# Kernel tuning notes

Measured on AMD Instinct MI355X. Metric: run time of the kernel, lower is better.

The kernel has to match this reference:

```python
import jax, jax.numpy as jnp
import numpy as np

NEG_SLOPE = 0.2

def gat_conv(x, edge_index, W, att_src, att_dst, bias, heads, out_dim):
    """PyG-style GATConv with add_self_loops=True, concat=True.
    x: [N, F_in]; edge_index: [2, E] with row 0 = src, row 1 = dst.
    W: [F_in, heads*out_dim]; att_src/att_dst: [heads, out_dim]; bias: [heads*out_dim].
    """
    N = x.shape[0]
    loop = jnp.arange(N)
    src = jnp.concatenate([edge_index[0], loop])  # [E+N]
    dst = jnp.concatenate([edge_index[1], loop])

    h = (x @ W).reshape(N, heads, out_dim)              # [N, H, D]
    a_s = jnp.sum(h * att_src[None], axis=-1)           # [N, H]
    a_d = jnp.sum(h * att_dst[None], axis=-1)           # [N, H]

    e = a_s[src] + a_d[dst]                             # [E+N, H]
    e = jax.nn.leaky_relu(e, NEG_SLOPE)
    # segment softmax over incoming edges of each dst node
    e_max = jax.ops.segment_max(e, dst, num_segments=N)  # [N, H]
    ex = jnp.exp(e - e_max[dst])
    denom = jax.ops.segment_sum(ex, dst, num_segments=N)  # [N, H] (>0: self loops)
    alpha = ex / denom[dst]                              # [E+N, H]

    msg = h[src] * alpha[..., None]                      # [E+N, H, D]
    out = jax.ops.segment_sum(msg, dst, num_segments=N)  # [N, H, D]
    return out.reshape(N, heads * out_dim) + bias


def setup_inputs() -> dict:
    key = jax.random.key(0)
    ks = jax.random.split(key, 16)
    N, F_in, D, H = 50000, 165, 64, 4
    E = 800000
    x = jax.random.normal(ks[0], (N, F_in), dtype=jnp.float32)
    edge_index = jax.random.randint(ks[1], (2, E), 0, N, dtype=jnp.int64)

    def glorot(k, shape):
        lim = float(np.sqrt(6.0 / (shape[0] + shape[-1])))
        return jax.random.uniform(k, shape, jnp.float32, -lim, lim)

    return {
        "x": x,
        "edge_index": edge_index,
        "proj_W": glorot(ks[2], (F_in, D)),
        "proj_b": jnp.zeros((D,), jnp.float32),
        "W1": glorot(ks[3], (D, H * D)),
        "att_src1": glorot(ks[4], (H, D)),
        "att_dst1": glorot(ks[5], (H, D)),
        "b1": jnp.zeros((H * D,), jnp.float32),
        "W2": glorot(ks[6], (H * D, D)),
        "att_src2": glorot(ks[7], (1, D)),
        "att_dst2": glorot(ks[8], (1, D)),
        "b2": jnp.zeros((D,), jnp.float32),
        "cls_W": glorot(ks[9], (D, 1)),
        "cls_b": jnp.zeros((1,), jnp.float32),
    }


def reference(x, edge_index, proj_W, proj_b, W1, att_src1, att_dst1, b1,
              W2, att_src2, att_dst2, b2, cls_W, cls_b):
    D = proj_W.shape[1]
    h = jax.nn.relu(x @ proj_W + proj_b)                              # [N, 64]
    h = jax.nn.relu(gat_conv(h, edge_index, W1, att_src1, att_dst1, b1, 4, D))   # [N, 256]
    h = jax.nn.relu(gat_conv(h, edge_index, W2, att_src2, att_dst2, b2, 1, D))   # [N, 64]
    return jnp.squeeze(h @ cls_W + cls_b, axis=-1)                    # [N]
```

## Files before the change

### kernel.cpp

```cpp
#include <hip/hip_runtime.h>

#define F_IN 165
#define KP_PROJ 168
constexpr float NEG_SLOPE = 0.2f;

__global__ void k_trans(const float* __restrict__ pw, const float* __restrict__ w2,
                        const float* __restrict__ w1, const float* __restrict__ as1w,
                        const float* __restrict__ ad1w,
                        float* __restrict__ t0, float* __restrict__ t2,
                        float* __restrict__ va) {
    int i = blockIdx.x * 256 + threadIdx.x;
    const int n0 = 64 * KP_PROJ, n2 = 64 * 256;
    if (i < n0) {
        int c = i / KP_PROJ, r = i - c * KP_PROJ;
        t0[i] = (r < F_IN) ? pw[r * 64 + c] : 0.f;
    } else if (i < n0 + n2) {
        int j = i - n0; int c = j >> 8, r = j & 255;
        t2[j] = w2[r * 64 + c];
    } else if (i < n0 + n2 + 512) {
        int j = i - n0 - n2;
        int i2 = j >> 6;
        int plane = i2 >> 2, h = i2 & 3, k = j & 63;
        const float* att = plane ? ad1w : as1w;
        float acc = 0.f;
        for (int c = 0; c < 64; ++c)
            acc = fmaf(w1[k * 256 + h * 64 + c], att[h * 64 + c], acc);
        va[j] = acc;
    }
}

__global__ void k_proj(const float* __restrict__ x, const float* __restrict__ Wt,
                       const float* __restrict__ b, float* __restrict__ h0, int N) {
    __shared__ float xs[32][KP_PROJ];
    int base = blockIdx.x * 32;
    int t = threadIdx.x;
    for (int idx = t; idx < 32 * KP_PROJ; idx += 256) {
        int nl = idx / KP_PROJ, k = idx - nl * KP_PROJ;
        int node = base + nl;
        xs[nl][k] = (node < N && k < F_IN) ? x[(size_t)node * F_IN + k] : 0.f;
    }
    __syncthreads();
    int g = t >> 6, col = t & 63;
    float acc[8];
    float bb = b[col];
#pragma unroll
    for (int m = 0; m < 8; ++m) acc[m] = bb;
    const float* wrow = Wt + col * KP_PROJ;
    for (int k4 = 0; k4 < KP_PROJ / 4; ++k4) {
        float4 wv = *(const float4*)(wrow + k4 * 4);
#pragma unroll
        for (int m = 0; m < 8; ++m) {
            float4 av = *(const float4*)&xs[g * 8 + m][k4 * 4];
            acc[m] = fmaf(av.x, wv.x, acc[m]);
            acc[m] = fmaf(av.y, wv.y, acc[m]);
            acc[m] = fmaf(av.z, wv.z, acc[m]);
            acc[m] = fmaf(av.w, wv.w, acc[m]);
        }
    }
#pragma unroll
    for (int m = 0; m < 8; ++m) {
        int node = base + g * 8 + m;
        if (node < N) h0[(size_t)node * 64 + col] = fmaxf(acc[m], 0.f);
    }
}

__global__ void k_attv1(const float* __restrict__ h0, const float* __restrict__ va,
                        float* __restrict__ as_, float* __restrict__ ad_, int N) {
    int t = threadIdx.x, lane = t & 63, wv = t >> 6;
    int n = blockIdx.x * 4 + wv;
    if (n >= N) return;
    float hv = h0[(size_t)n * 64 + lane];
    float r0 = hv * va[0 * 64 + lane], r1 = hv * va[1 * 64 + lane];
    float r2 = hv * va[2 * 64 + lane], r3 = hv * va[3 * 64 + lane];
    float r4 = hv * va[4 * 64 + lane], r5 = hv * va[5 * 64 + lane];
    float r6 = hv * va[6 * 64 + lane], r7 = hv * va[7 * 64 + lane];
#pragma unroll
    for (int off = 32; off; off >>= 1) {
        r0 += __shfl_xor(r0, off, 64); r1 += __shfl_xor(r1, off, 64);
        r2 += __shfl_xor(r2, off, 64); r3 += __shfl_xor(r3, off, 64);
        r4 += __shfl_xor(r4, off, 64); r5 += __shfl_xor(r5, off, 64);
        r6 += __shfl_xor(r6, off, 64); r7 += __shfl_xor(r7, off, 64);
    }
    if (lane == 0) {
        *(float4*)(as_ + (size_t)n * 4) = make_float4(r0, r1, r2, r3);
        *(float4*)(ad_ + (size_t)n * 4) = make_float4(r4, r5, r6, r7);
    }
}

__global__ void k_lin2(const float* __restrict__ h1, const float* __restrict__ Wt,
                       const float* __restrict__ att_s, const float* __restrict__ att_d,
                       float* __restrict__ out, float* __restrict__ as_,
                       float* __restrict__ ad_, int N) {
    __shared__ float hs[32][256];
    int base = blockIdx.x * 32;
    int t = threadIdx.x;
    for (int i = 0; i < 8; ++i) {
        int idx4 = t + i * 256;
        int nl = idx4 >> 6, k4 = idx4 & 63;
        int node = base + nl;
        float4 v = make_float4(0.f, 0.f, 0.f, 0.f);
        if (node < N) v = *(const float4*)(h1 + (size_t)node * 256 + k4 * 4);
        *(float4*)&hs[nl][k4 * 4] = v;
    }
    __syncthreads();
    int g = t >> 6, col = t & 63;
    float acc[8] = {};
    const float* wrow = Wt + col * 256;
    for (int k4 = 0; k4 < 64; ++k4) {
        float4 wv = *(const float4*)(wrow + k4 * 4);
#pragma unroll
        for (int m = 0; m < 8; ++m) {
            float4 av = *(const float4*)&hs[g * 8 + m][k4 * 4];
            acc[m] = fmaf(av.x, wv.x, acc[m]);
            acc[m] = fmaf(av.y, wv.y, acc[m]);
            acc[m] = fmaf(av.z, wv.z, acc[m]);
            acc[m] = fmaf(av.w, wv.w, acc[m]);
        }
    }
    float sw = att_s[col], dw = att_d[col];
#pragma unroll
    for (int m = 0; m < 8; ++m) {
        int node = base + g * 8 + m;
        if (node < N) out[(size_t)node * 64 + col] = acc[m];
        float sv = acc[m] * sw, dv = acc[m] * dw;
#pragma unroll
        for (int off = 32; off; off >>= 1) {
            sv += __shfl_xor(sv, off, 64);
            dv += __shfl_xor(dv, off, 64);
        }
        if (col == 0 && node < N) { as_[node] = sv; ad_[node] = dv; }
    }
}

__global__ void k_deg(const int* __restrict__ ei, int E, int N, int* __restrict__ deg) {
    int total = E + N;
    for (int i = blockIdx.x * blockDim.x + threadIdx.x; i < total; i += gridDim.x * blockDim.x) {
        int dst = (i < E) ? ei[E + i] : (i - E);
        atomicAdd(&deg[dst], 1);
    }
}

__global__ void k_scan_part(const int* __restrict__ deg, int* __restrict__ out,
                            int* __restrict__ partials, int n) {
    __shared__ int tmp[1024];
    int b = blockIdx.x, t = threadIdx.x;
    int i = b * 1024 + t;
    int v = (i < n) ? deg[i] : 0;
    tmp[t] = v;
    __syncthreads();
    for (int off = 1; off < 1024; off <<= 1) {
        int xval = (t >= off) ? tmp[t - off] : 0;
        __syncthreads();
        tmp[t] += xval;
        __syncthreads();
    }
    if (i < n) out[i] = tmp[t] - v;
    if (t == 1023) partials[b] = tmp[t];
}

__global__ void k_scan_small(int* __restrict__ partials, int nblk) {
    int lane = threadIdx.x & 63;
    int carry = 0;
    for (int base = 0; base < nblk; base += 64) {
        int idx = base + lane;
        int v = (idx < nblk) ? partials[idx] : 0;
        int orig = v;
#pragma unroll
        for (int off = 1; off < 64; off <<= 1) {
            int u = __shfl_up(v, off, 64);
            if (lane >= off) v += u;
        }
        if (idx < nblk) partials[idx] = carry + v - orig;
        carry += __shfl(v, 63, 64);
    }
}

__global__ void k_scan_add(int* __restrict__ rowptr, const int* __restrict__ partials,
                           int n, int total) {
    int i = blockIdx.x * 1024 + threadIdx.x;
    if (i < n) rowptr[i] += partials[blockIdx.x];
    if (i == 0) rowptr[n] = total;
}

__global__ void k_scatter(const int* __restrict__ ei, int E, int N,
                          const int* __restrict__ rowptr, int* __restrict__ cursor,
                          int* __restrict__ csrc) {
    int total = E + N;
    for (int i = blockIdx.x * blockDim.x + threadIdx.x; i < total; i += gridDim.x * blockDim.x) {
        int src, dst;
        if (i < E) { src = ei[i]; dst = ei[E + i]; }
        else { src = i - E; dst = i - E; }
        int pos = rowptr[dst] + atomicAdd(&cursor[dst], 1);
        csrc[pos] = src;
    }
}

__global__ void k_gat1f(const float* __restrict__ h0, const float* __restrict__ as1,
                        const float* __restrict__ ad1, const int* __restrict__ rowptr,
                        const int* __restrict__ csrc, const float* __restrict__ W1,
                        const float* __restrict__ b1, float* __restrict__ h1out, int N) {
    __shared__ float agg[4][256];
    int t = threadIdx.x, wv = t >> 6, lane = t & 63;
    int slot = lane >> 4, sl = lane & 15;
    int d = blockIdx.x * 4 + wv;
    if (d < N) {
        int s0 = rowptr[d], e0 = rowptr[d + 1];
        float4 ad = *(const float4*)(ad1 + (size_t)d * 4);
        float a00=0,a01=0,a02=0,a03=0;
        float a10=0,a11=0,a12=0,a13=0;
        float a20=0,a21=0,a22=0,a23=0;
        float a30=0,a31=0,a32=0,a33=0;
        float d0=0,d1=0,d2=0,d3=0;
        const float* hb = h0 + sl * 4;
        for (int j = s0 + slot; j < e0; j += 4) {
            int s = csrc[j];
            float4 a = *(const float4*)(as1 + (size_t)s * 4);
            float4 hv = *(const float4*)(hb + (size_t)s * 64);
            float z0 = a.x + ad.x, z1 = a.y + ad.y, z2 = a.z + ad.z, z3 = a.w + ad.w;
            z0 = (z0 > 0.f) ? z0 : NEG_SLOPE * z0;
            z1 = (z1 > 0.f) ? z1 : NEG_SLOPE * z1;
            z2 = (z2 > 0.f) ? z2 : NEG_SLOPE * z2;
            z3 = (z3 > 0.f) ? z3 : NEG_SLOPE * z3;
            float wx = __expf(z0), wy = __expf(z1), wz = __expf(z2), ww = __expf(z3);
            a00 = fmaf(wx, hv.x, a00); a01 = fmaf(wx, hv.y, a01);
            a02 = fmaf(wx, hv.z, a02); a03 = fmaf(wx, hv.w, a03);
            a10 = fmaf(wy, hv.x, a10); a11 = fmaf(wy, hv.y, a11);
            a12 = fmaf(wy, hv.z, a12); a13 = fmaf(wy, hv.w, a13);
            a20 = fmaf(wz, hv.x, a20); a21 = fmaf(wz, hv.y, a21);
            a22 = fmaf(wz, hv.z, a22); a23 = fmaf(wz, hv.w, a23);
            a30 = fmaf(ww, hv.x, a30); a31 = fmaf(ww, hv.y, a31);
            a32 = fmaf(ww, hv.z, a32); a33 = fmaf(ww, hv.w, a33);
            d0 += wx; d1 += wy; d2 += wz; d3 += ww;
        }
#pragma unroll
        for (int off = 16; off <= 32; off <<= 1) {
            a00 += __shfl_xor(a00, off, 64); a01 += __shfl_xor(a01, off, 64);
            a02 += __shfl_xor(a02, off, 64); a03 += __shfl_xor(a03, off, 64);
            a10 += __shfl_xor(a10, off, 64); a11 += __shfl_xor(a11, off, 64);
            a12 += __shfl_xor(a12, off, 64); a13 += __shfl_xor(a13, off, 64);
            a20 += __shfl_xor(a20, off, 64); a21 += __shfl_xor(a21, off, 64);
            a22 += __shfl_xor(a22, off, 64); a23 += __shfl_xor(a23, off, 64);
            a30 += __shfl_xor(a30, off, 64); a31 += __shfl_xor(a31, off, 64);
            a32 += __shfl_xor(a32, off, 64); a33 += __shfl_xor(a33, off, 64);
            d0  += __shfl_xor(d0,  off, 64); d1  += __shfl_xor(d1,  off, 64);
            d2  += __shfl_xor(d2,  off, 64); d3  += __shfl_xor(d3,  off, 64);
        }
        if (slot == 0) {
            float i0 = 1.f / d0, i1 = 1.f / d1, i2 = 1.f / d2, i3 = 1.f / d3;
            *(float4*)&agg[wv][  0 + sl * 4] = make_float4(a00*i0, a01*i0, a02*i0, a03*i0);
            *(float4*)&agg[wv][ 64 + sl * 4] = make_float4(a10*i1, a11*i1, a12*i1, a13*i1);
            *(float4*)&agg[wv][128 + sl * 4] = make_float4(a20*i2, a21*i2, a22*i2, a23*i2);
            *(float4*)&agg[wv][192 + sl * 4] = make_float4(a30*i3, a31*i3, a32*i3, a33*i3);
        }
    }
    __syncthreads();
    int h = t >> 6;
    float o0 = 0.f, o1 = 0.f, o2 = 0.f, o3 = 0.f;
    for (int k = 0; k < 64; ++k) {
        float wv1 = W1[k * 256 + t];
        o0 = fmaf(agg[0][h * 64 + k], wv1, o0);
        o1 = fmaf(agg[1][h * 64 + k], wv1, o1);
        o2 = fmaf(agg[2][h * 64 + k], wv1, o2);
        o3 = fmaf(agg[3][h * 64 + k], wv1, o3);
    }
    float bb = b1[t];
    int base = blockIdx.x * 4;
    if (base + 0 < N) h1out[(size_t)(base + 0) * 256 + t] = fmaxf(o0 + bb, 0.f);
    if (base + 1 < N) h1out[(size_t)(base + 1) * 256 + t] = fmaxf(o1 + bb, 0.f);
    if (base + 2 < N) h1out[(size_t)(base + 2) * 256 + t] = fmaxf(o2 + bb, 0.f);
    if (base + 3 < N) h1out[(size_t)(base + 3) * 256 + t] = fmaxf(o3 + bb, 0.f);
}

__global__ void k_gat2(const float* __restrict__ hlin, const float* __restrict__ as2,
                       const float* __restrict__ ad2, const int* __restrict__ rowptr,
                       const int* __restrict__ csrc, const float* __restrict__ bias,
                       const float* __restrict__ clsW, const float* __restrict__ clsB,
                       float* __restrict__ out, int N) {
    int t = threadIdx.x, wv = t >> 6, lane = t & 63;
    int slot = lane >> 4, sl = lane & 15;
    int d = blockIdx.x * 4 + wv;
    if (d >= N) return;
    int s0 = rowptr[d], e0 = rowptr[d + 1];
    float add = ad2[d];
    float ax = 0.f, ay = 0.f, az = 0.f, aw = 0.f, den = 0.f;
    const float* hb = hlin + sl * 4;
    for (int j = s0 + slot; j < e0; j += 4) {
        int s = csrc[j];
        float z = as2[s] + add;
        z = (z > 0.f) ? z : NEG_SLOPE * z;
        float w = __expf(z);
        float4 hv = *(const float4*)(hb + (size_t)s * 64);
        ax = fmaf(w, hv.x, ax); ay = fmaf(w, hv.y, ay);
        az = fmaf(w, hv.z, az); aw = fmaf(w, hv.w, aw);
        den += w;
    }
#pragma unroll
    for (int off = 16; off <= 32; off <<= 1) {
        ax += __shfl_xor(ax, off, 64); ay += __shfl_xor(ay, off, 64);
        az += __shfl_xor(az, off, 64); aw += __shfl_xor(aw, off, 64);
        den += __shfl_xor(den, off, 64);
    }
    float inv = 1.f / den;
    float4 bb = *(const float4*)(bias + sl * 4);
    float4 cw = *(const float4*)(clsW + sl * 4);
    float p = fmaxf(fmaf(ax, inv, bb.x), 0.f) * cw.x
            + fmaxf(fmaf(ay, inv, bb.y), 0.f) * cw.y
            + fmaxf(fmaf(az, inv, bb.z), 0.f) * cw.z
            + fmaxf(fmaf(aw, inv, bb.w), 0.f) * cw.w;
#pragma unroll
    for (int off = 1; off <= 8; off <<= 1) p += __shfl_xor(p, off, 64);
    if (lane == 0) out[d] = p + clsB[0];
}

extern "C" void kernel_launch(void* const* d_in, const int* in_sizes, int n_in,
                              void* d_out, int out_size, void* d_ws, size_t ws_size,
                              hipStream_t stream) {
    const float* x     = (const float*)d_in[0];
    const int*   ei    = (const int*)d_in[1];
    const float* projW = (const float*)d_in[2];
    const float* projB = (const float*)d_in[3];
    const float* W1    = (const float*)d_in[4];
    const float* as1w  = (const float*)d_in[5];
    const float* ad1w  = (const float*)d_in[6];
    const float* b1    = (const float*)d_in[7];
    const float* W2    = (const float*)d_in[8];
    const float* as2w  = (const float*)d_in[9];
    const float* ad2w  = (const float*)d_in[10];
    const float* b2    = (const float*)d_in[11];
    const float* clsW  = (const float*)d_in[12];
    const float* clsB  = (const float*)d_in[13];
    float* out = (float*)d_out;

    const int N = in_sizes[0] / F_IN;
    const int E = in_sizes[1] / 2;
    const int total = E + N;

    char* ws = (char*)d_ws;
    size_t off = 0;
    auto alloc = [&](size_t bytes) -> void* {
        void* p = ws + off;
        off += (bytes + 255) & ~(size_t)255;
        return p;
    };
    float* h0     = (float*)alloc((size_t)N * 64 * 4);
    float* h1     = (float*)alloc((size_t)N * 256 * 4);
    float* as1    = (float*)alloc((size_t)N * 4 * 4);
    float* ad1    = (float*)alloc((size_t)N * 4 * 4);
    float* as2    = (float*)alloc((size_t)N * 4);
    float* ad2    = (float*)alloc((size_t)N * 4);
    int*   deg    = (int*)alloc((size_t)N * 4);
    int*   rowptr = (int*)alloc((size_t)(N + 1) * 4);
    int*   cursor = (int*)alloc((size_t)N * 4);
    int*   parts  = (int*)alloc(1024 * 4);
    int*   csrc   = (int*)alloc((size_t)total * 4);
    float* wt0    = (float*)alloc(64 * KP_PROJ * 4);
    float* wt2    = (float*)alloc(64 * 256 * 4);
    float* va     = (float*)alloc(512 * 4);
    float* h2lin  = h0;

    k_trans<<<(64 * KP_PROJ + 64 * 256 + 512 + 255) / 256, 256, 0, stream>>>(
        projW, W2, W1, as1w, ad1w, wt0, wt2, va);

    hipMemsetAsync(deg, 0, (size_t)N * 4, stream);
    hipMemsetAsync(cursor, 0, (size_t)N * 4, stream);
    k_deg<<<1024, 256, 0, stream>>>(ei, E, N, deg);
    int nblk = (N + 1023) / 1024;
    k_scan_part<<<nblk, 1024, 0, stream>>>(deg, rowptr, parts, N);
    k_scan_small<<<1, 64, 0, stream>>>(parts, nblk);
    k_scan_add<<<nblk, 1024, 0, stream>>>(rowptr, parts, N, total);
    k_scatter<<<1024, 256, 0, stream>>>(ei, E, N, rowptr, cursor, csrc);

    k_proj<<<(N + 31) / 32, 256, 0, stream>>>(x, wt0, projB, h0, N);

    k_attv1<<<(N + 3) / 4, 256, 0, stream>>>(h0, va, as1, ad1, N);
    k_gat1f<<<(N + 3) / 4, 256, 0, stream>>>(h0, as1, ad1, rowptr, csrc, W1, b1, h1, N);

    k_lin2<<<(N + 31) / 32, 256, 0, stream>>>(h1, wt2, as2w, ad2w, h2lin, as2, ad2, N);
    k_gat2<<<(N + 3) / 4, 256, 0, stream>>>(h2lin, as2, ad2, rowptr, csrc, b2,
                                            clsW, clsB, out, N);
}
```

Measured before the change: 342.8 us.

## Handle self-loops implicitly in GAT kernels and merge degree/cursor memsets

Self-loop edges are no longer added to the CSR. Each GAT aggregation kernel now seeds the slot-0 accumulator with the node's own contribution, which removes N atomics from the degree and scatter passes and shrinks the column array. The deg and cursor buffers now share one allocation, so a single memset clears both. The gat1 shared aggregation buffer is re-laid out per head with an unrolled k-loop to change LDS access patterns. This costs four times more shared memory there, and rowptr totals now count only E.

```diff
diff --git a/kernel.cpp b/kernel.cpp
--- a/kernel.cpp
+++ b/kernel.cpp
@@ -132,11 +132,9 @@
     }
 }
 
-__global__ void k_deg(const int* __restrict__ ei, int E, int N, int* __restrict__ deg) {
-    int total = E + N;
-    for (int i = blockIdx.x * blockDim.x + threadIdx.x; i < total; i += gridDim.x * blockDim.x) {
-        int dst = (i < E) ? ei[E + i] : (i - E);
-        atomicAdd(&deg[dst], 1);
+__global__ void k_deg(const int* __restrict__ ei, int E, int* __restrict__ deg) {
+    for (int i = blockIdx.x * blockDim.x + threadIdx.x; i < E; i += gridDim.x * blockDim.x) {
+        atomicAdd(&deg[ei[E + i]], 1);
     }
 }
 
@@ -182,14 +180,11 @@
     if (i == 0) rowptr[n] = total;
 }
 
-__global__ void k_scatter(const int* __restrict__ ei, int E, int N,
+__global__ void k_scatter(const int* __restrict__ ei, int E,
                           const int* __restrict__ rowptr, int* __restrict__ cursor,
                           int* __restrict__ csrc) {
-    int total = E + N;
-    for (int i = blockIdx.x * blockDim.x + threadIdx.x; i < total; i += gridDim.x * blockDim.x) {
-        int src, dst;
-        if (i < E) { src = ei[i]; dst = ei[E + i]; }
-        else { src = i - E; dst = i - E; }
+    for (int i = blockIdx.x * blockDim.x + threadIdx.x; i < E; i += gridDim.x * blockDim.x) {
+        int src = ei[i], dst = ei[E + i];
         int pos = rowptr[dst] + atomicAdd(&cursor[dst], 1);
         csrc[pos] = src;
     }
@@ -199,7 +194,7 @@
                         const float* __restrict__ ad1, const int* __restrict__ rowptr,
                         const int* __restrict__ csrc, const float* __restrict__ W1,
                         const float* __restrict__ b1, float* __restrict__ h1out, int N) {
-    __shared__ float agg[4][256];
+    __shared__ float agg2[4][256][4];
     int t = threadIdx.x, wv = t >> 6, lane = t & 63;
     int slot = lane >> 4, sl = lane & 15;
     int d = blockIdx.x * 4 + wv;
@@ -212,6 +207,21 @@
         float a30=0,a31=0,a32=0,a33=0;
         float d0=0,d1=0,d2=0,d3=0;
         const float* hb = h0 + sl * 4;
+        if (slot == 0) {
+            float4 a = *(const float4*)(as1 + (size_t)d * 4);
+            float z0 = a.x + ad.x, z1 = a.y + ad.y, z2 = a.z + ad.z, z3 = a.w + ad.w;
+            z0 = (z0 > 0.f) ? z0 : NEG_SLOPE * z0;
+            z1 = (z1 > 0.f) ? z1 : NEG_SLOPE * z1;
+            z2 = (z2 > 0.f) ? z2 : NEG_SLOPE * z2;
+            z3 = (z3 > 0.f) ? z3 : NEG_SLOPE * z3;
+            float wx = __expf(z0), wy = __expf(z1), wz = __expf(z2), ww = __expf(z3);
+            float4 hv = *(const float4*)(hb + (size_t)d * 64);
+            a00 = wx*hv.x; a01 = wx*hv.y; a02 = wx*hv.z; a03 = wx*hv.w;
+            a10 = wy*hv.x; a11 = wy*hv.y; a12 = wy*hv.z; a13 = wy*hv.w;
+            a20 = wz*hv.x; a21 = wz*hv.y; a22 = wz*hv.z; a23 = wz*hv.w;
+            a30 = ww*hv.x; a31 = ww*hv.y; a32 = ww*hv.z; a33 = ww*hv.w;
+            d0 = wx; d1 = wy; d2 = wz; d3 = ww;
+        }
         for (int j = s0 + slot; j < e0; j += 4) {
             int s = csrc[j];
             float4 a = *(const float4*)(as1 + (size_t)s * 4);
@@ -247,21 +257,27 @@
         }
         if (slot == 0) {
             float i0 = 1.f / d0, i1 = 1.f / d1, i2 = 1.f / d2, i3 = 1.f / d3;
-            *(float4*)&agg[wv][  0 + sl * 4] = make_float4(a00*i0, a01*i0, a02*i0, a03*i0);
-            *(float4*)&agg[wv][ 64 + sl * 4] = make_float4(a10*i1, a11*i1, a12*i1, a13*i1);
-            *(float4*)&agg[wv][128 + sl * 4] = make_float4(a20*i2, a21*i2, a22*i2, a23*i2);
-            *(float4*)&agg[wv][192 + sl * 4] = make_float4(a30*i3, a31*i3, a32*i3, a33*i3);
+            int kb = sl * 4;
+            agg2[wv][  0 + kb][0] = a00*i0; agg2[wv][  0 + kb + 1][0] = a01*i0;
+            agg2[wv][  0 + kb + 2][0] = a02*i0; agg2[wv][  0 + kb + 3][0] = a03*i0;
+            agg2[wv][ 64 + kb][1] = a10*i1; agg2[wv][ 64 + kb + 1][1] = a11*i1;
+            agg2[wv][ 64 + kb + 2][1] = a12*i1; agg2[wv][ 64 + kb + 3][1] = a13*i1;
+            agg2[wv][128 + kb][2] = a20*i2; agg2[wv][128 + kb + 1][2] = a21*i2;
+            agg2[wv][128 + kb + 2][2] = a22*i2; agg2[wv][128 + kb + 3][2] = a23*i2;
+            agg2[wv][192 + kb][3] = a30*i3; agg2[wv][192 + kb + 1][3] = a31*i3;
+            agg2[wv][192 + kb + 2][3] = a32*i3; agg2[wv][192 + kb + 3][3] = a33*i3;
         }
     }
     __syncthreads();
     int h = t >> 6;
     float o0 = 0.f, o1 = 0.f, o2 = 0.f, o3 = 0.f;
+#pragma unroll 4
     for (int k = 0; k < 64; ++k) {
         float wv1 = W1[k * 256 + t];
-        o0 = fmaf(agg[0][h * 64 + k], wv1, o0);
-        o1 = fmaf(agg[1][h * 64 + k], wv1, o1);
-        o2 = fmaf(agg[2][h * 64 + k], wv1, o2);
-        o3 = fmaf(agg[3][h * 64 + k], wv1, o3);
+        o0 = fmaf(agg2[0][h * 64 + k][h], wv1, o0);
+        o1 = fmaf(agg2[1][h * 64 + k][h], wv1, o1);
+        o2 = fmaf(agg2[2][h * 64 + k][h], wv1, o2);
+        o3 = fmaf(agg2[3][h * 64 + k][h], wv1, o3);
     }
     float bb = b1[t];
     int base = blockIdx.x * 4;
@@ -284,6 +300,14 @@
     float add = ad2[d];
     float ax = 0.f, ay = 0.f, az = 0.f, aw = 0.f, den = 0.f;
     const float* hb = hlin + sl * 4;
+    if (slot == 0) {
+        float z = as2[d] + add;
+        z = (z > 0.f) ? z : NEG_SLOPE * z;
+        float w = __expf(z);
+        float4 hv = *(const float4*)(hb + (size_t)d * 64);
+        ax = w * hv.x; ay = w * hv.y; az = w * hv.z; aw = w * hv.w;
+        den = w;
+    }
     for (int j = s0 + slot; j < e0; j += 4) {
         int s = csrc[j];
         float z = as2[s] + add;
@@ -333,7 +357,6 @@
 
     const int N = in_sizes[0] / F_IN;
     const int E = in_sizes[1] / 2;
-    const int total = E + N;
 
     char* ws = (char*)d_ws;
     size_t off = 0;
@@ -348,11 +371,12 @@
     float* ad1    = (float*)alloc((size_t)N * 4 * 4);
     float* as2    = (float*)alloc((size_t)N * 4);
     float* ad2    = (float*)alloc((size_t)N * 4);
-    int*   deg    = (int*)alloc((size_t)N * 4);
+    int*   dc     = (int*)alloc((size_t)2 * N * 4);
+    int*   deg    = dc;
+    int*   cursor = dc + N;
     int*   rowptr = (int*)alloc((size_t)(N + 1) * 4);
-    int*   cursor = (int*)alloc((size_t)N * 4);
     int*   parts  = (int*)alloc(1024 * 4);
-    int*   csrc   = (int*)alloc((size_t)total * 4);
+    int*   csrc   = (int*)alloc((size_t)E * 4);
     float* wt0    = (float*)alloc(64 * KP_PROJ * 4);
     float* wt2    = (float*)alloc(64 * 256 * 4);
     float* va     = (float*)alloc(512 * 4);
@@ -361,14 +385,13 @@
     k_trans<<<(64 * KP_PROJ + 64 * 256 + 512 + 255) / 256, 256, 0, stream>>>(
         projW, W2, W1, as1w, ad1w, wt0, wt2, va);
 
-    hipMemsetAsync(deg, 0, (size_t)N * 4, stream);
-    hipMemsetAsync(cursor, 0, (size_t)N * 4, stream);
-    k_deg<<<1024, 256, 0, stream>>>(ei, E, N, deg);
+    hipMemsetAsync(dc, 0, (size_t)2 * N * 4, stream);
+    k_deg<<<1024, 256, 0, stream>>>(ei, E, deg);
     int nblk = (N + 1023) / 1024;
     k_scan_part<<<nblk, 1024, 0, stream>>>(deg, rowptr, parts, N);
     k_scan_small<<<1, 64, 0, stream>>>(parts, nblk);
-    k_scan_add<<<nblk, 1024, 0, stream>>>(rowptr, parts, N, total);
-    k_scatter<<<1024, 256, 0, stream>>>(ei, E, N, rowptr, cursor, csrc);
+    k_scan_add<<<nblk, 1024, 0, stream>>>(rowptr, parts, N, E);
+    k_scatter<<<1024, 256, 0, stream>>>(ei, E, rowptr, cursor, csrc);
 
     k_proj<<<(N + 31) / 32, 256, 0, stream>>>(x, wt0, projB, h0, N);
 
```

Result: no change. 347.8 us (+1.5%).
